# Kernel optimization log

Hardware: AMD Instinct MI355X
Metric: run time of the kernel (lower is better)

The kernel has to match this reference:

```python
import jax, jax.numpy as jnp
import numpy as np

MIN_NORM = 1e-15
BALL_EPS = 4e-3  # fp32 boundary eps used by PoincareBall.proj


def _artanh(x):
    x = jnp.clip(x, -1.0 + 1e-7, 1.0 - 1e-7)
    return 0.5 * (jnp.log1p(x) - jnp.log1p(-x))


def _norm(x):
    return jnp.maximum(jnp.linalg.norm(x, axis=-1, keepdims=True), MIN_NORM)


def mobius_matvec(m, x, c):
    sqrt_c = jnp.sqrt(c)
    x_norm = _norm(x)
    mx = x @ m  # [N, out]
    mx_norm = _norm(mx)
    res_c = jnp.tanh(mx_norm / x_norm * _artanh(sqrt_c * x_norm)) * mx / (mx_norm * sqrt_c)
    cond = jnp.all(mx == 0, axis=-1, keepdims=True)
    return jnp.where(cond, jnp.zeros((), dtype=x.dtype), res_c)


def expmap0(u, c):
    sqrt_c = jnp.sqrt(c)
    u_norm = _norm(u)
    return jnp.tanh(sqrt_c * u_norm) * u / (sqrt_c * u_norm)


def logmap0(p, c):
    sqrt_c = jnp.sqrt(c)
    p_norm = _norm(p)
    return _artanh(sqrt_c * p_norm) * p / (sqrt_c * p_norm)


def proj(x, c):
    norm = _norm(x)
    maxnorm = (1.0 - BALL_EPS) / jnp.sqrt(c)
    return jnp.where(norm > maxnorm, x / norm * maxnorm, x)


def mobius_add(x, y, c):
    x2 = jnp.sum(x * x, axis=-1, keepdims=True)
    y2 = jnp.sum(y * y, axis=-1, keepdims=True)
    xy = jnp.sum(x * y, axis=-1, keepdims=True)
    num = (1.0 + 2.0 * c * xy + c * y2) * x + (1.0 - c * x2) * y
    denom = 1.0 + 2.0 * c * xy + c * c * x2 * y2
    return num / jnp.maximum(denom, MIN_NORM)


def setup_inputs() -> dict:
    key = jax.random.key(0)
    N, E, IN, OUT = 50000, 800000, 256, 64
    ks = jax.random.split(key, 6)
    x = jax.random.normal(ks[0], (N, IN), dtype=jnp.float32) * 0.1
    weight = jax.random.normal(ks[1], (IN, OUT), dtype=jnp.float32) / np.sqrt(IN)
    bias = jax.random.normal(ks[2], (OUT,), dtype=jnp.float32) * 0.01
    vals = jax.random.uniform(ks[3], (E,), dtype=jnp.float32) / 16.0  # ~normalized adj
    row = jax.random.randint(ks[4], (E,), 0, N, dtype=jnp.int32)
    col = jax.random.randint(ks[5], (E,), 0, N, dtype=jnp.int32)
    c = jnp.asarray(1.0, dtype=jnp.float32)
    return {"x": x, "weight": weight, "bias": bias, "vals": vals, "c": c, "row": row, "col": col}


def reference(x, weight, bias, vals, c, row, col):
    N = x.shape[0]
    out = mobius_matvec(weight, x, c)
    # proj_tan0 is identity on the Poincare ball
    hyp_bias = proj(expmap0(bias[None, :], c), c)
    out = mobius_add(out, hyp_bias, c)
    out = logmap0(out, c)
    # sparse.mm(adj, out): gather neighbor rows, weight by edge vals, scatter-add
    out = jax.ops.segment_sum(vals[:, None] * out[col], row, num_segments=N)
    out = proj(expmap0(out, c), c)
    return out
```

## Files before the change

### kernel.cpp

```cpp
#include <hip/hip_runtime.h>
#include <math.h>

#define MIN_NORM 1e-15f
#define BALL_EPS 4e-3f

typedef __attribute__((ext_vector_type(8))) short bf16x8;
typedef __attribute__((ext_vector_type(4))) float f32x4;

__device__ __forceinline__ short f2bf(float f) {
  unsigned u = __builtin_bit_cast(unsigned, f);
  u = u + 0x7FFFu + ((u >> 16) & 1u);
  return (short)(u >> 16);
}
__device__ __forceinline__ float bf2f(unsigned short us) {
  unsigned u = ((unsigned)us) << 16;
  return __builtin_bit_cast(float, u);
}

__device__ __forceinline__ float wsum(float v) {
#pragma unroll
  for (int off = 32; off; off >>= 1) v += __shfl_xor(v, off, 64);
  return v;
}

__device__ __forceinline__ float artanh_clip(float z) {
  z = fminf(fmaxf(z, -1.0f + 1e-7f), 1.0f - 1e-7f);
  return 0.5f * (log1pf(z) - log1pf(-z));
}

__global__ __launch_bounds__(256) void k1_gemm_hist(
    const float* __restrict__ x, const float* __restrict__ W,
    float* __restrict__ mx_ws, float* __restrict__ x2_ws, int N,
    const int* __restrict__ row, int* __restrict__ cnt, int E, int G1) {
  if ((int)blockIdx.x >= G1) {
    const int nb = gridDim.x - G1;
    for (int i = (blockIdx.x - G1) * 256 + threadIdx.x; i < E; i += nb * 256)
      atomicAdd(&cnt[row[i]], 1);
    return;
  }
  const int lane = threadIdx.x & 63;
  const int wid = threadIdx.x >> 6;
  const int m = lane & 15;
  const int g = lane >> 4;

  bf16x8 b[8][4];
#pragma unroll
  for (int kk = 0; kk < 8; ++kk)
#pragma unroll
    for (int t = 0; t < 4; ++t) {
      const float* wp = &W[(kk * 32 + g * 8) * 64 + t * 16 + m];
      bf16x8 bb;
#pragma unroll
      for (int j = 0; j < 8; ++j) bb[j] = f2bf(wp[j * 64]);
      b[kk][t] = bb;
    }

  const int nb16 = (N + 15) >> 4;
  const int wstep = G1 * 4;
  for (int rb = blockIdx.x * 4 + wid; rb < nb16; rb += wstep) {
    int arow = rb * 16 + m;
    if (arow >= N) arow = N - 1;
    const float* xp = &x[(size_t)arow * 256 + g * 8];

    bf16x8 a[8];
    float x2p = 0.f;
#pragma unroll
    for (int kk = 0; kk < 8; ++kk) {
      float4 v0 = *(const float4*)(xp + kk * 32);
      float4 v1 = *(const float4*)(xp + kk * 32 + 4);
      x2p += v0.x * v0.x + v0.y * v0.y + v0.z * v0.z + v0.w * v0.w +
             v1.x * v1.x + v1.y * v1.y + v1.z * v1.z + v1.w * v1.w;
      bf16x8 aa;
      aa[0] = f2bf(v0.x); aa[1] = f2bf(v0.y); aa[2] = f2bf(v0.z); aa[3] = f2bf(v0.w);
      aa[4] = f2bf(v1.x); aa[5] = f2bf(v1.y); aa[6] = f2bf(v1.z); aa[7] = f2bf(v1.w);
      a[kk] = aa;
    }
    float x2f = x2p;
    x2f += __shfl_xor(x2f, 16, 64);
    x2f += __shfl_xor(x2f, 32, 64);

    f32x4 acc[4];
#pragma unroll
    for (int t = 0; t < 4; ++t) { acc[t][0] = 0.f; acc[t][1] = 0.f; acc[t][2] = 0.f; acc[t][3] = 0.f; }
#pragma unroll
    for (int kk = 0; kk < 8; ++kk)
#pragma unroll
      for (int t = 0; t < 4; ++t)
        acc[t] = __builtin_amdgcn_mfma_f32_16x16x32_bf16(a[kk], b[kk][t], acc[t], 0, 0, 0);

#pragma unroll
    for (int j = 0; j < 4; ++j) {
      int orow = rb * 16 + g * 4 + j;
      if (orow < N) {
        float* mp = &mx_ws[(size_t)orow * 64 + m];
#pragma unroll
        for (int t = 0; t < 4; ++t) mp[t * 16] = acc[t][j];
      }
    }
    if (g == 0 && rb * 16 + m < N) x2_ws[rb * 16 + m] = x2f;
  }
}

__global__ __launch_bounds__(256) void k1b_hyp(
    const float* __restrict__ mx_ws, const float* __restrict__ x2_ws,
    const float* __restrict__ bias, const float* __restrict__ cptr,
    unsigned short* __restrict__ h, int N) {
  const int lane = threadIdx.x & 63;
  const int wid = threadIdx.x >> 6;
  const int sub = lane >> 4;
  const int q = lane & 15;
  const float c = *cptr;
  const float sc = sqrtf(c);
  const float maxnorm = (1.0f - BALL_EPS) / sc;

  float4 bv = *(const float4*)&bias[q * 4];
  float bsq = bv.x * bv.x + bv.y * bv.y + bv.z * bv.z + bv.w * bv.w;
#pragma unroll
  for (int o = 1; o < 16; o <<= 1) bsq += __shfl_xor(bsq, o, 64);
  float bnorm = fmaxf(sqrtf(bsq), MIN_NORM);
  float tb = tanhf(sc * bnorm);
  float bfac = tb / (sc * bnorm);
  float hbn = fmaxf(tb / sc, MIN_NORM);
  float pfac = (hbn > maxnorm) ? (maxnorm / hbn) : 1.0f;
  float hb0 = bv.x * bfac * pfac, hb1 = bv.y * bfac * pfac;
  float hb2 = bv.z * bfac * pfac, hb3 = bv.w * bfac * pfac;
  float y2 = hb0 * hb0 + hb1 * hb1 + hb2 * hb2 + hb3 * hb3;
#pragma unroll
  for (int o = 1; o < 16; o <<= 1) y2 += __shfl_xor(y2, o, 64);

  const int r = (blockIdx.x * 4 + wid) * 4 + sub;
  if (r >= N) return;

  float4 mv = *(const float4*)&mx_ws[(size_t)r * 64 + q * 4];
  float x2v = x2_ws[r];

  float msq = mv.x * mv.x + mv.y * mv.y + mv.z * mv.z + mv.w * mv.w;
  int z = (mv.x == 0.f) && (mv.y == 0.f) && (mv.z == 0.f) && (mv.w == 0.f);
#pragma unroll
  for (int o = 1; o < 16; o <<= 1) {
    msq += __shfl_xor(msq, o, 64);
    z &= __shfl_xor(z, o, 64);
  }
  float mx_norm = fmaxf(sqrtf(msq), MIN_NORM);
  float x_norm = fmaxf(sqrtf(x2v), MIN_NORM);
  float art = artanh_clip(sc * x_norm);
  float tt = tanhf(mx_norm / x_norm * art);
  float fac = z ? 0.f : (tt / (mx_norm * sc));
  float r0 = mv.x * fac, r1 = mv.y * fac, r2 = mv.z * fac, r3 = mv.w * fac;

  float x2m = r0 * r0 + r1 * r1 + r2 * r2 + r3 * r3;
  float xy = r0 * hb0 + r1 * hb1 + r2 * hb2 + r3 * hb3;
#pragma unroll
  for (int o = 1; o < 16; o <<= 1) {
    x2m += __shfl_xor(x2m, o, 64);
    xy += __shfl_xor(xy, o, 64);
  }
  float k2 = 1.f + 2.f * c * xy;
  float ca = k2 + c * y2;
  float cb = 1.f - c * x2m;
  float inv = 1.f / fmaxf(k2 + c * c * x2m * y2, MIN_NORM);
  float a0 = (ca * r0 + cb * hb0) * inv;
  float a1 = (ca * r1 + cb * hb1) * inv;
  float a2 = (ca * r2 + cb * hb2) * inv;
  float a3 = (ca * r3 + cb * hb3) * inv;

  float psq = a0 * a0 + a1 * a1 + a2 * a2 + a3 * a3;
#pragma unroll
  for (int o = 1; o < 16; o <<= 1) psq += __shfl_xor(psq, o, 64);
  float p_norm = fmaxf(sqrtf(psq), MIN_NORM);
  float art2 = artanh_clip(sc * p_norm);
  float fac2 = art2 / (sc * p_norm);

  ushort4 hv;
  hv.x = (unsigned short)f2bf(a0 * fac2);
  hv.y = (unsigned short)f2bf(a1 * fac2);
  hv.z = (unsigned short)f2bf(a2 * fac2);
  hv.w = (unsigned short)f2bf(a3 * fac2);
  *(ushort4*)&h[(size_t)r * 64 + q * 4] = hv;
}

__global__ __launch_bounds__(1024) void scan_a(const int* __restrict__ cnt,
                                               int* __restrict__ rowptr,
                                               int* __restrict__ blksum, int N) {
  __shared__ int wsums[16];
  int gid = blockIdx.x * 1024 + threadIdx.x;
  int lane = threadIdx.x & 63, w = threadIdx.x >> 6;
  int v = (gid < N) ? cnt[gid] : 0;
  int s = v;
#pragma unroll
  for (int d = 1; d < 64; d <<= 1) { int t = __shfl_up(s, d, 64); if (lane >= d) s += t; }
  if (lane == 63) wsums[w] = s;
  __syncthreads();
  if (w == 0 && lane < 16) {
    int ss = wsums[lane];
#pragma unroll
    for (int d = 1; d < 16; d <<= 1) { int u = __shfl_up(ss, d, 64); if (lane >= d) ss += u; }
    wsums[lane] = ss;
  }
  __syncthreads();
  if (w > 0) s += wsums[w - 1];
  if (gid < N) rowptr[1 + gid] = s;
  if (threadIdx.x == 1023) blksum[blockIdx.x] = s;
}

__global__ __launch_bounds__(1024) void scan_c(int* __restrict__ rowptr,
                                               const int* __restrict__ blksum,
                                               int N, int nblk) {
  __shared__ int s_off;
  if (threadIdx.x < 64) {
    int acc = 0;
    for (int bidx = threadIdx.x; bidx < (int)blockIdx.x; bidx += 64) acc += blksum[bidx];
#pragma unroll
    for (int off = 32; off; off >>= 1) acc += __shfl_xor(acc, off, 64);
    if (threadIdx.x == 0) s_off = acc;
  }
  __syncthreads();
  int gid = blockIdx.x * 1024 + threadIdx.x;
  if (gid == 0) rowptr[0] = 0;
  if (gid < N) rowptr[1 + gid] += s_off;
}

__global__ __launch_bounds__(256) void scatter_kernel(
    const int* __restrict__ row, const int* __restrict__ col,
    const float* __restrict__ vals, int* __restrict__ rowptr,
    int2* __restrict__ pairs, int E) {
  int i = blockIdx.x * blockDim.x + threadIdx.x;
  if (i < E) {
    int r = row[i];
    int pos = atomicAdd(&rowptr[r], 1);
    pairs[pos] = make_int2(col[i], __builtin_bit_cast(int, vals[i]));
  }
}

__global__ __launch_bounds__(256) void segsum_kernel(
    const unsigned short* __restrict__ h, const int* __restrict__ rowptr,
    const int2* __restrict__ pairs, const float* __restrict__ cptr,
    float* __restrict__ out, int N) {
  const int lane = threadIdx.x & 63;
  const int wid = threadIdx.x >> 6;
  const int sw = lane >> 4;
  const int q = lane & 15;
  int r = blockIdx.x * 4 + wid;
  if (r >= N) return;
  const float c = *cptr;
  const float sc = sqrtf(c);
  const float maxnorm = (1.0f - BALL_EPS) / sc;
  int st = (r > 0) ? rowptr[r - 1] : 0;
  int en = rowptr[r];
  st = __builtin_amdgcn_readfirstlane(st);
  en = __builtin_amdgcn_readfirstlane(en);

  float a0 = 0.f, a1 = 0.f, a2 = 0.f, a3 = 0.f;
#pragma unroll 2
  for (int i = st + sw; i < en; i += 4) {
    int2 pv = pairs[i];
    float vv = __builtin_bit_cast(float, pv.y);
    ushort4 hv = *(const ushort4*)&h[(size_t)pv.x * 64 + q * 4];
    a0 = fmaf(vv, bf2f(hv.x), a0);
    a1 = fmaf(vv, bf2f(hv.y), a1);
    a2 = fmaf(vv, bf2f(hv.z), a2);
    a3 = fmaf(vv, bf2f(hv.w), a3);
  }
  a0 += __shfl_xor(a0, 32, 64); a1 += __shfl_xor(a1, 32, 64);
  a2 += __shfl_xor(a2, 32, 64); a3 += __shfl_xor(a3, 32, 64);
  a0 += __shfl_xor(a0, 16, 64); a1 += __shfl_xor(a1, 16, 64);
  a2 += __shfl_xor(a2, 16, 64); a3 += __shfl_xor(a3, 16, 64);

  float sq = a0 * a0 + a1 * a1 + a2 * a2 + a3 * a3;
#pragma unroll
  for (int o = 1; o < 16; o <<= 1) sq += __shfl_xor(sq, o, 64);
  float un = fmaxf(sqrtf(sq), MIN_NORM);
  float th = tanhf(sc * un);
  float fac = th / (sc * un);
  float p0 = a0 * fac, p1 = a1 * fac, p2 = a2 * fac, p3 = a3 * fac;
  float psq = p0 * p0 + p1 * p1 + p2 * p2 + p3 * p3;
#pragma unroll
  for (int o = 1; o < 16; o <<= 1) psq += __shfl_xor(psq, o, 64);
  float pn = fmaxf(sqrtf(psq), MIN_NORM);
  if (pn > maxnorm) {
    float pf = maxnorm / pn;
    p0 *= pf; p1 *= pf; p2 *= pf; p3 *= pf;
  }
  if (sw == 0)
    *(float4*)&out[(size_t)r * 64 + q * 4] = make_float4(p0, p1, p2, p3);
}

__global__ __launch_bounds__(256) void edge_kernel(
    const unsigned short* __restrict__ h, const float* __restrict__ vals,
    const int* __restrict__ row, const int* __restrict__ col,
    float* __restrict__ out, int E) {
  const int lane = threadIdx.x & 63;
  const int wid0 = (blockIdx.x * blockDim.x + threadIdx.x) >> 6;
  const int nw = (gridDim.x * blockDim.x) >> 6;
  for (int e = wid0; e < E; e += nw) {
    int eu = __builtin_amdgcn_readfirstlane(e);
    float v = vals[eu];
    int r = row[eu];
    int cl = col[eu];
    atomicAdd(&out[(size_t)r * 64 + lane], v * bf2f(h[(size_t)cl * 64 + lane]));
  }
}

__global__ __launch_bounds__(256) void final_kernel(
    float* __restrict__ out, const float* __restrict__ cptr, int N) {
  const int lane = threadIdx.x & 63;
  const int wid0 = (blockIdx.x * blockDim.x + threadIdx.x) >> 6;
  const int nw = (gridDim.x * blockDim.x) >> 6;
  const float c = *cptr;
  const float sc = sqrtf(c);
  const float maxnorm = (1.0f - BALL_EPS) / sc;
  for (int r = wid0; r < N; r += nw) {
    float u = out[(size_t)r * 64 + lane];
    float un = fmaxf(sqrtf(wsum(u * u)), MIN_NORM);
    float th = tanhf(sc * un);
    float p = th * u / (sc * un);
    float pn = fmaxf(sqrtf(wsum(p * p)), MIN_NORM);
    if (pn > maxnorm) p = p / pn * maxnorm;
    out[(size_t)r * 64 + lane] = p;
  }
}

static inline size_t align256(size_t x) { return (x + 255) & ~(size_t)255; }

extern "C" void kernel_launch(void* const* d_in, const int* in_sizes, int n_in,
                              void* d_out, int out_size, void* d_ws, size_t ws_size,
                              hipStream_t stream) {
  const float* x = (const float*)d_in[0];
  const float* W = (const float*)d_in[1];
  const float* bias = (const float*)d_in[2];
  const float* vals = (const float*)d_in[3];
  const float* cptr = (const float*)d_in[4];
  const int* row = (const int*)d_in[5];
  const int* col = (const int*)d_in[6];
  float* out = (float*)d_out;

  const int OUT = in_sizes[2];
  const int IN = in_sizes[1] / OUT;
  const int N = in_sizes[0] / IN;
  const int E = in_sizes[3];

  char* ws = (char*)d_ws;
  size_t o_mx = 0;
  size_t o_h = align256(o_mx + (size_t)N * 64 * 4);
  size_t o_x2 = align256(o_h + (size_t)N * 64 * 2);
  size_t o_rowptr = align256(o_x2 + (size_t)N * 4);
  size_t o_blk = align256(o_rowptr + (size_t)(N + 1) * 4);
  size_t o_cnt = align256(o_blk + 1024 * 4);
  size_t needed = o_cnt + (size_t)N * 4;
  bool pairs_fit = (size_t)E * 8 <= o_h;

  float* mx_ws = (float*)(ws + o_mx);
  unsigned short* h = (unsigned short*)(ws + o_h);
  float* x2_ws = (float*)(ws + o_x2);

  const int nb16 = (N + 15) / 16;
  const int G1 = (nb16 + 7) / 8;
  const int HB = 256;
  const int k1b_blocks = (N + 15) / 16;

  if (needed <= ws_size && pairs_fit) {
    int* rowptr = (int*)(ws + o_rowptr);
    int* blksum = (int*)(ws + o_blk);
    int* cnt = (int*)(ws + o_cnt);
    int2* pairs = (int2*)(ws + o_mx);

    const int nblk = (N + 1023) / 1024;
    const int eb = (E + 255) / 256;

    hipMemsetAsync(cnt, 0, (size_t)N * 4, stream);
    k1_gemm_hist<<<G1 + HB, 256, 0, stream>>>(x, W, mx_ws, x2_ws, N, row, cnt, E, G1);
    k1b_hyp<<<k1b_blocks, 256, 0, stream>>>(mx_ws, x2_ws, bias, cptr, h, N);
    scan_a<<<nblk, 1024, 0, stream>>>(cnt, rowptr, blksum, N);
    scan_c<<<nblk, 1024, 0, stream>>>(rowptr, blksum, N, nblk);
    scatter_kernel<<<eb, 256, 0, stream>>>(row, col, vals, rowptr, pairs, E);
    segsum_kernel<<<(N + 3) / 4, 256, 0, stream>>>(h, rowptr, pairs, cptr, out, N);
  } else {
    k1_gemm_hist<<<G1, 256, 0, stream>>>(x, W, mx_ws, x2_ws, N, row, (int*)nullptr, 0, G1);
    k1b_hyp<<<k1b_blocks, 256, 0, stream>>>(mx_ws, x2_ws, bias, cptr, h, N);
    hipMemsetAsync(d_out, 0, (size_t)out_size * sizeof(float), stream);
    edge_kernel<<<2048, 256, 0, stream>>>(h, vals, row, col, out, E);
    final_kernel<<<1024, 256, 0, stream>>>(out, cptr, N);
  }
}
```

Before: 227.3 us.

## Replace per-row CSR build with coarse row-bucket binning and LDS accumulation

```diff
diff --git a/kernel.cpp b/kernel.cpp
--- a/kernel.cpp
+++ b/kernel.cpp
@@ -3,6 +3,9 @@
 
 #define MIN_NORM 1e-15f
 #define BALL_EPS 4e-3f
+#define BSH 7
+#define BW  128
+#define NBMAX 512
 
 typedef __attribute__((ext_vector_type(8))) short bf16x8;
 typedef __attribute__((ext_vector_type(4))) float f32x4;
@@ -28,14 +31,39 @@
   return 0.5f * (log1pf(z) - log1pf(-z));
 }
 
-__global__ __launch_bounds__(256) void k1_gemm_hist(
-    const float* __restrict__ x, const float* __restrict__ W,
+__global__ __launch_bounds__(256) void kprep(
+    const float* __restrict__ W, unsigned short* __restrict__ w_frag,
+    int* __restrict__ bucket_total) {
+  if (blockIdx.x == 16) {
+    for (int i = threadIdx.x; i < NBMAX; i += 256) bucket_total[i] = 0;
+    return;
+  }
+  int base = blockIdx.x * 256 + threadIdx.x;
+#pragma unroll
+  for (int r = 0; r < 4; ++r) {
+    int o = base + r * 4096;
+    int j = o & 7, m = (o >> 3) & 15, g = (o >> 7) & 3, t = (o >> 9) & 3, kk = o >> 11;
+    w_frag[o] = (unsigned short)f2bf(W[(kk * 32 + g * 8 + j) * 64 + t * 16 + m]);
+  }
+}
+
+__global__ __launch_bounds__(256) void k1_gemm_count(
+    const float* __restrict__ x, const unsigned short* __restrict__ w_frag,
     float* __restrict__ mx_ws, float* __restrict__ x2_ws, int N,
-    const int* __restrict__ row, int* __restrict__ cnt, int E, int G1) {
+    const int* __restrict__ row, int* __restrict__ bucket_total, int E,
+    int G1, int ECHUNK) {
   if ((int)blockIdx.x >= G1) {
-    const int nb = gridDim.x - G1;
-    for (int i = (blockIdx.x - G1) * 256 + threadIdx.x; i < E; i += nb * 256)
-      atomicAdd(&cnt[row[i]], 1);
+    __shared__ int lhist[NBMAX];
+    int cb = blockIdx.x - G1;
+    for (int i = threadIdx.x; i < NBMAX; i += 256) lhist[i] = 0;
+    __syncthreads();
+    int st = cb * ECHUNK;
+    int en = min(E, st + ECHUNK);
+    for (int i = st + (int)threadIdx.x; i < en; i += 256)
+      atomicAdd(&lhist[row[i] >> BSH], 1);
+    __syncthreads();
+    for (int i = threadIdx.x; i < NBMAX; i += 256)
+      if (lhist[i]) atomicAdd(&bucket_total[i], lhist[i]);
     return;
   }
   const int lane = threadIdx.x & 63;
@@ -47,13 +75,8 @@
 #pragma unroll
   for (int kk = 0; kk < 8; ++kk)
 #pragma unroll
-    for (int t = 0; t < 4; ++t) {
-      const float* wp = &W[(kk * 32 + g * 8) * 64 + t * 16 + m];
-      bf16x8 bb;
-#pragma unroll
-      for (int j = 0; j < 8; ++j) bb[j] = f2bf(wp[j * 64]);
-      b[kk][t] = bb;
-    }
+    for (int t = 0; t < 4; ++t)
+      b[kk][t] = *(const bf16x8*)&w_frag[(size_t)((kk * 4 + t) * 64 + lane) * 8];
 
   const int nb16 = (N + 15) >> 4;
   const int wstep = G1 * 4;
@@ -101,10 +124,29 @@
   }
 }
 
-__global__ __launch_bounds__(256) void k1b_hyp(
+__global__ __launch_bounds__(256) void k2_hyp_scan(
     const float* __restrict__ mx_ws, const float* __restrict__ x2_ws,
     const float* __restrict__ bias, const float* __restrict__ cptr,
-    unsigned short* __restrict__ h, int N) {
+    unsigned short* __restrict__ h, int N, int k1bBlocks,
+    const int* __restrict__ bucket_total, int* __restrict__ gbase,
+    int* __restrict__ gcursor, int NB) {
+  if ((int)blockIdx.x >= k1bBlocks) {
+    if (threadIdx.x < 64) {
+      int tid = threadIdx.x;
+      int running = 0;
+      for (int kk = 0; kk < 8; ++kk) {
+        int idx = kk * 64 + tid;
+        int v = (idx < NB) ? bucket_total[idx] : 0;
+        int s = v;
+#pragma unroll
+        for (int d = 1; d < 64; d <<= 1) { int t = __shfl_up(s, d, 64); if (tid >= d) s += t; }
+        if (idx < NB) { int ex = running + s - v; gbase[idx] = ex; gcursor[idx] = ex; }
+        running += __shfl(s, 63, 64);
+      }
+      if (tid == 0) gbase[NB] = running;
+    }
+    return;
+  }
   const int lane = threadIdx.x & 63;
   const int wid = threadIdx.x >> 6;
   const int sub = lane >> 4;
@@ -179,110 +221,116 @@
   *(ushort4*)&h[(size_t)r * 64 + q * 4] = hv;
 }
 
-__global__ __launch_bounds__(1024) void scan_a(const int* __restrict__ cnt,
-                                               int* __restrict__ rowptr,
-                                               int* __restrict__ blksum, int N) {
-  __shared__ int wsums[16];
-  int gid = blockIdx.x * 1024 + threadIdx.x;
-  int lane = threadIdx.x & 63, w = threadIdx.x >> 6;
-  int v = (gid < N) ? cnt[gid] : 0;
-  int s = v;
-#pragma unroll
-  for (int d = 1; d < 64; d <<= 1) { int t = __shfl_up(s, d, 64); if (lane >= d) s += t; }
-  if (lane == 63) wsums[w] = s;
-  __syncthreads();
-  if (w == 0 && lane < 16) {
-    int ss = wsums[lane];
-#pragma unroll
-    for (int d = 1; d < 16; d <<= 1) { int u = __shfl_up(ss, d, 64); if (lane >= d) ss += u; }
-    wsums[lane] = ss;
-  }
-  __syncthreads();
-  if (w > 0) s += wsums[w - 1];
-  if (gid < N) rowptr[1 + gid] = s;
-  if (threadIdx.x == 1023) blksum[blockIdx.x] = s;
-}
-
-__global__ __launch_bounds__(1024) void scan_c(int* __restrict__ rowptr,
-                                               const int* __restrict__ blksum,
-                                               int N, int nblk) {
-  __shared__ int s_off;
-  if (threadIdx.x < 64) {
-    int acc = 0;
-    for (int bidx = threadIdx.x; bidx < (int)blockIdx.x; bidx += 64) acc += blksum[bidx];
-#pragma unroll
-    for (int off = 32; off; off >>= 1) acc += __shfl_xor(acc, off, 64);
-    if (threadIdx.x == 0) s_off = acc;
-  }
-  __syncthreads();
-  int gid = blockIdx.x * 1024 + threadIdx.x;
-  if (gid == 0) rowptr[0] = 0;
-  if (gid < N) rowptr[1 + gid] += s_off;
-}
-
-__global__ __launch_bounds__(256) void scatter_kernel(
+__global__ __launch_bounds__(256) void k3_binscatter(
     const int* __restrict__ row, const int* __restrict__ col,
-    const float* __restrict__ vals, int* __restrict__ rowptr,
-    int2* __restrict__ pairs, int E) {
-  int i = blockIdx.x * blockDim.x + threadIdx.x;
-  if (i < E) {
-    int r = row[i];
-    int pos = atomicAdd(&rowptr[r], 1);
-    pairs[pos] = make_int2(col[i], __builtin_bit_cast(int, vals[i]));
-  }
-}
-
-__global__ __launch_bounds__(256) void segsum_kernel(
-    const unsigned short* __restrict__ h, const int* __restrict__ rowptr,
-    const int2* __restrict__ pairs, const float* __restrict__ cptr,
+    const float* __restrict__ vals, int* __restrict__ gcursor,
+    uint2* __restrict__ bins, int E, int NB) {
+  __shared__ uint2 stag[4096];
+  __shared__ int dstoff[4096];
+  __shared__ int hist[NBMAX], lbase[NBMAX], off[NBMAX];
+  const int tid = threadIdx.x;
+  const int st = blockIdx.x * 4096;
+  const int n = min(4096, E - st);
+  for (int i = tid; i < NBMAX; i += 256) hist[i] = 0;
+  __syncthreads();
+  for (int i = tid; i < n; i += 256) atomicAdd(&hist[row[st + i] >> BSH], 1);
+  __syncthreads();
+  if (tid < 64) {
+    int running = 0;
+    for (int k = 0; k < 8; ++k) {
+      int idx = k * 64 + tid;
+      int v = hist[idx];
+      int s = v;
+#pragma unroll
+      for (int d = 1; d < 64; d <<= 1) { int t = __shfl_up(s, d, 64); if (tid >= d) s += t; }
+      lbase[idx] = running + s - v;
+      running += __shfl(s, 63, 64);
+    }
+  }
+  __syncthreads();
+  for (int b = tid; b < NB; b += 256) {
+    int cnt = hist[b];
+    int go = cnt ? atomicAdd(&gcursor[b], cnt) : 0;
+    off[b] = go - lbase[b];
+  }
+  __syncthreads();
+  for (int i = tid; i < NBMAX; i += 256) hist[i] = 0;
+  __syncthreads();
+  for (int i = tid; i < n; i += 256) {
+    int r = row[st + i];
+    int b = r >> BSH;
+    unsigned meta = ((unsigned)(r & (BW - 1)) << 16) | (unsigned)col[st + i];
+    int rank = atomicAdd(&hist[b], 1);
+    int slot = lbase[b] + rank;
+    stag[slot] = make_uint2(meta, __builtin_bit_cast(unsigned, vals[st + i]));
+    dstoff[slot] = off[b];
+  }
+  __syncthreads();
+  for (int i = tid; i < n; i += 256) bins[dstoff[i] + i] = stag[i];
+}
+
+__global__ __launch_bounds__(256) void k4_binsum(
+    const unsigned short* __restrict__ h, const uint2* __restrict__ bins,
+    const int* __restrict__ gbase, const float* __restrict__ cptr,
     float* __restrict__ out, int N) {
-  const int lane = threadIdx.x & 63;
-  const int wid = threadIdx.x >> 6;
-  const int sw = lane >> 4;
+  __shared__ float acc[BW * 64];
+  const int tid = threadIdx.x;
+  const int lane = tid & 63;
+  const int wid = tid >> 6;
+  const int g = wid * 4 + (lane >> 4);
   const int q = lane & 15;
-  int r = blockIdx.x * 4 + wid;
-  if (r >= N) return;
+  const int k = q >> 3;
+  const int qq = q & 7;
+  const int b = blockIdx.x;
+  for (int i = tid * 4; i < BW * 64; i += 1024)
+    *(float4*)&acc[i] = make_float4(0.f, 0.f, 0.f, 0.f);
+  __syncthreads();
+  int st = gbase[b], en = gbase[b + 1];
+  st = __builtin_amdgcn_readfirstlane(st);
+  en = __builtin_amdgcn_readfirstlane(en);
+
+#define PROC(EE)                                                            \
+  {                                                                         \
+    uint2 rec = bins[EE];                                                   \
+    unsigned cc = rec.x & 0xFFFFu;                                          \
+    unsigned rowl = rec.x >> 16;                                            \
+    float v = __builtin_bit_cast(float, rec.y);                             \
+    bf16x8 hv = *(const bf16x8*)&h[(size_t)cc * 64 + qq * 8];               \
+    float* ap = &acc[rowl * 64 + qq * 8];                                   \
+    _Pragma("unroll")                                                       \
+    for (int j = 0; j < 8; ++j)                                             \
+      atomicAdd(ap + j, v * bf2f((unsigned short)hv[j]));                   \
+  }
+
+  int e = st + g * 2 + k;
+  for (; e + 32 < en; e += 64) { PROC(e); PROC(e + 32); }
+  if (e < en) PROC(e);
+#undef PROC
+  __syncthreads();
+
   const float c = *cptr;
   const float sc = sqrtf(c);
   const float maxnorm = (1.0f - BALL_EPS) / sc;
-  int st = (r > 0) ? rowptr[r - 1] : 0;
-  int en = rowptr[r];
-  st = __builtin_amdgcn_readfirstlane(st);
-  en = __builtin_amdgcn_readfirstlane(en);
-
-  float a0 = 0.f, a1 = 0.f, a2 = 0.f, a3 = 0.f;
-#pragma unroll 2
-  for (int i = st + sw; i < en; i += 4) {
-    int2 pv = pairs[i];
-    float vv = __builtin_bit_cast(float, pv.y);
-    ushort4 hv = *(const ushort4*)&h[(size_t)pv.x * 64 + q * 4];
-    a0 = fmaf(vv, bf2f(hv.x), a0);
-    a1 = fmaf(vv, bf2f(hv.y), a1);
-    a2 = fmaf(vv, bf2f(hv.z), a2);
-    a3 = fmaf(vv, bf2f(hv.w), a3);
-  }
-  a0 += __shfl_xor(a0, 32, 64); a1 += __shfl_xor(a1, 32, 64);
-  a2 += __shfl_xor(a2, 32, 64); a3 += __shfl_xor(a3, 32, 64);
-  a0 += __shfl_xor(a0, 16, 64); a1 += __shfl_xor(a1, 16, 64);
-  a2 += __shfl_xor(a2, 16, 64); a3 += __shfl_xor(a3, 16, 64);
-
-  float sq = a0 * a0 + a1 * a1 + a2 * a2 + a3 * a3;
-#pragma unroll
-  for (int o = 1; o < 16; o <<= 1) sq += __shfl_xor(sq, o, 64);
-  float un = fmaxf(sqrtf(sq), MIN_NORM);
-  float th = tanhf(sc * un);
-  float fac = th / (sc * un);
-  float p0 = a0 * fac, p1 = a1 * fac, p2 = a2 * fac, p3 = a3 * fac;
-  float psq = p0 * p0 + p1 * p1 + p2 * p2 + p3 * p3;
-#pragma unroll
-  for (int o = 1; o < 16; o <<= 1) psq += __shfl_xor(psq, o, 64);
-  float pn = fmaxf(sqrtf(psq), MIN_NORM);
-  if (pn > maxnorm) {
-    float pf = maxnorm / pn;
-    p0 *= pf; p1 *= pf; p2 *= pf; p3 *= pf;
-  }
-  if (sw == 0)
-    *(float4*)&out[(size_t)r * 64 + q * 4] = make_float4(p0, p1, p2, p3);
+#pragma unroll
+  for (int it = 0; it < BW / 16; ++it) {
+    int rl = it * 16 + g;
+    int grow = b * BW + rl;
+    float4 a = *(float4*)&acc[rl * 64 + q * 4];
+    float sq = a.x * a.x + a.y * a.y + a.z * a.z + a.w * a.w;
+#pragma unroll
+    for (int o = 1; o < 16; o <<= 1) sq += __shfl_xor(sq, o, 64);
+    float un = fmaxf(sqrtf(sq), MIN_NORM);
+    float th = tanhf(sc * un);
+    float fac = th / (sc * un);
+    float p0 = a.x * fac, p1 = a.y * fac, p2 = a.z * fac, p3 = a.w * fac;
+    float psq = p0 * p0 + p1 * p1 + p2 * p2 + p3 * p3;
+#pragma unroll
+    for (int o = 1; o < 16; o <<= 1) psq += __shfl_xor(psq, o, 64);
+    float pn = fmaxf(sqrtf(psq), MIN_NORM);
+    if (pn > maxnorm) { float pf = maxnorm / pn; p0 *= pf; p1 *= pf; p2 *= pf; p3 *= pf; }
+    if (grow < N)
+      *(float4*)&out[(size_t)grow * 64 + q * 4] = make_float4(p0, p1, p2, p3);
+  }
 }
 
 __global__ __launch_bounds__(256) void edge_kernel(
@@ -340,43 +388,51 @@
   const int E = in_sizes[3];
 
   char* ws = (char*)d_ws;
-  size_t o_mx = 0;
-  size_t o_h = align256(o_mx + (size_t)N * 64 * 4);
-  size_t o_x2 = align256(o_h + (size_t)N * 64 * 2);
-  size_t o_rowptr = align256(o_x2 + (size_t)N * 4);
-  size_t o_blk = align256(o_rowptr + (size_t)(N + 1) * 4);
-  size_t o_cnt = align256(o_blk + 1024 * 4);
-  size_t needed = o_cnt + (size_t)N * 4;
-  bool pairs_fit = (size_t)E * 8 <= o_h;
-
+  size_t o_wf = 0;
+  size_t o_mx = align256(o_wf + 16384 * 2);
+  size_t o_x2 = align256(o_mx + (size_t)N * 64 * 4);
+  size_t o_h = align256(o_x2 + (size_t)N * 4);
+  size_t o_bt = align256(o_h + (size_t)N * 64 * 2);
+  size_t o_gb = align256(o_bt + NBMAX * 4);
+  size_t o_gc = align256(o_gb + (NBMAX + 1) * 4);
+  size_t needed = o_gc + NBMAX * 4;
+
+  unsigned short* w_frag = (unsigned short*)(ws + o_wf);
   float* mx_ws = (float*)(ws + o_mx);
+  float* x2_ws = (float*)(ws + o_x2);
   unsigned short* h = (unsigned short*)(ws + o_h);
-  float* x2_ws = (float*)(ws + o_x2);
-
+  int* bucket_total = (int*)(ws + o_bt);
+  int* gbase = (int*)(ws + o_gb);
+  int* gcursor = (int*)(ws + o_gc);
+  uint2* bins = (uint2*)(ws + o_mx);
+
+  const int NB = (N + BW - 1) / BW;
   const int nb16 = (N + 15) / 16;
-  const int G1 = (nb16 + 7) / 8;
-  const int HB = 256;
-  const int k1b_blocks = (N + 15) / 16;
-
-  if (needed <= ws_size && pairs_fit) {
-    int* rowptr = (int*)(ws + o_rowptr);
-    int* blksum = (int*)(ws + o_blk);
-    int* cnt = (int*)(ws + o_cnt);
-    int2* pairs = (int2*)(ws + o_mx);
-
-    const int nblk = (N + 1023) / 1024;
-    const int eb = (E + 255) / 256;
-
-    hipMemsetAsync(cnt, 0, (size_t)N * 4, stream);
-    k1_gemm_hist<<<G1 + HB, 256, 0, stream>>>(x, W, mx_ws, x2_ws, N, row, cnt, E, G1);
-    k1b_hyp<<<k1b_blocks, 256, 0, stream>>>(mx_ws, x2_ws, bias, cptr, h, N);
-    scan_a<<<nblk, 1024, 0, stream>>>(cnt, rowptr, blksum, N);
-    scan_c<<<nblk, 1024, 0, stream>>>(rowptr, blksum, N, nblk);
-    scatter_kernel<<<eb, 256, 0, stream>>>(row, col, vals, rowptr, pairs, E);
-    segsum_kernel<<<(N + 3) / 4, 256, 0, stream>>>(h, rowptr, pairs, cptr, out, N);
+  const int G1 = 782;
+  const int CB = 100;
+  const int ECHUNK = (E + CB - 1) / CB;
+  const int k1bBlocks = (N + 15) / 16;
+
+  bool fast = (needed <= ws_size) && (N <= 65536) && (NB <= NBMAX) &&
+              ((size_t)E * 8 <= (size_t)N * 256) && (E > 0);
+
+  if (fast) {
+    kprep<<<17, 256, 0, stream>>>(W, w_frag, bucket_total);
+    k1_gemm_count<<<G1 + CB, 256, 0, stream>>>(x, w_frag, mx_ws, x2_ws, N,
+                                               row, bucket_total, E, G1, ECHUNK);
+    k2_hyp_scan<<<k1bBlocks + 1, 256, 0, stream>>>(mx_ws, x2_ws, bias, cptr, h, N,
+                                                   k1bBlocks, bucket_total, gbase,
+                                                   gcursor, NB);
+    k3_binscatter<<<(E + 4095) / 4096, 256, 0, stream>>>(row, col, vals, gcursor,
+                                                         bins, E, NB);
+    k4_binsum<<<NB, 256, 0, stream>>>(h, bins, gbase, cptr, out, N);
   } else {
-    k1_gemm_hist<<<G1, 256, 0, stream>>>(x, W, mx_ws, x2_ws, N, row, (int*)nullptr, 0, G1);
-    k1b_hyp<<<k1b_blocks, 256, 0, stream>>>(mx_ws, x2_ws, bias, cptr, h, N);
+    kprep<<<17, 256, 0, stream>>>(W, w_frag, bucket_total);
+    k1_gemm_count<<<G1, 256, 0, stream>>>(x, w_frag, mx_ws, x2_ws, N,
+                                          row, (int*)nullptr, 0, G1, ECHUNK);
+    k2_hyp_scan<<<k1bBlocks, 256, 0, stream>>>(mx_ws, x2_ws, bias, cptr, h, N,
+                                               k1bBlocks + 1, bucket_total, gbase,
+                                               gcursor, NB);
     hipMemsetAsync(d_out, 0, (size_t)out_size * sizeof(float), stream);
     edge_kernel<<<2048, 256, 0, stream>>>(h, vals, row, col, out, E);
     final_kernel<<<1024, 256, 0, stream>>>(out, cptr, N);
```

Result: slower. 503.5 us (+121.5%).
